# Kernel tuning notes

Hardware: AMD Instinct MI355X
Metric: run time of the kernel (lower is better)

Reference implementation:

```python
import jax, jax.numpy as jnp
import numpy as np

ALPHA_SIZE = 256
EMBED_DIM = 256
HIDDEN = 1024
BATCH = 64
SEQ = 512
TEMPERATURE = 1.0


def setup_inputs() -> dict:
    key = jax.random.key(0)
    ks = jax.random.split(key, 10)
    s = 0.05  # keep activations in a sane range
    return {
        "x": jax.random.randint(ks[0], (BATCH, SEQ), 0, ALPHA_SIZE, dtype=jnp.int32),
        "emb": jax.random.normal(ks[1], (ALPHA_SIZE, EMBED_DIM), jnp.float32) * s,
        "W0": jax.random.normal(ks[2], (EMBED_DIM, 3 * HIDDEN), jnp.float32) * s,
        "U0": jax.random.normal(ks[3], (HIDDEN, 3 * HIDDEN), jnp.float32) * s,
        "b0": jax.random.normal(ks[4], (2, 3 * HIDDEN), jnp.float32) * s,
        "W1": jax.random.normal(ks[5], (HIDDEN, 3 * HIDDEN), jnp.float32) * s,
        "U1": jax.random.normal(ks[6], (HIDDEN, 3 * HIDDEN), jnp.float32) * s,
        "b1": jax.random.normal(ks[7], (2, 3 * HIDDEN), jnp.float32) * s,
        "Wd": jax.random.normal(ks[8], (HIDDEN, ALPHA_SIZE), jnp.float32) * s,
        "bd": jax.random.normal(ks[9], (ALPHA_SIZE,), jnp.float32) * s,
        "training": 0,
    }


def gru_layer(x, W, U, b):
    # Keras GRU, reset_after=True, gate order (z, r, h). x: [B,S,D]
    B, S, _ = x.shape
    H = U.shape[0]
    # precompute input-side gates for all timesteps: [B,S,3H]
    xg = jnp.einsum("bsd,dg->bsg", x, W) + b[0]

    def step(h, xg_t):
        hg = h @ U + b[1]  # [B,3H]
        xz, xr, xh = jnp.split(xg_t, 3, axis=-1)
        hz, hr, hh_r = jnp.split(hg, 3, axis=-1)
        z = jax.nn.sigmoid(xz + hz)
        r = jax.nn.sigmoid(xr + hr)
        hh = jnp.tanh(xh + r * hh_r)
        h_new = z * h + (1.0 - z) * hh
        return h_new, h_new

    h0 = jnp.zeros((B, H), x.dtype)
    _, ys = jax.lax.scan(step, h0, jnp.swapaxes(xg, 0, 1))  # [S,B,H]
    return jnp.swapaxes(ys, 0, 1)  # [B,S,H]


def reference(x, emb, W0, U0, b0, W1, U1, b1, Wd, bd, training):
    h = emb[x]  # [B,S,E]
    h = gru_layer(h, W0, U0, b0)
    h = gru_layer(h, W1, U1, b1)
    logits = jnp.einsum("bsh,hv->bsv", h, Wd) + bd
    if not training:
        logits = logits / TEMPERATURE
    return jax.nn.softmax(logits, axis=-1)
```

## Files before the change

### kernel.cpp

```cpp
#include <hip/hip_runtime.h>

typedef _Float16 half_t;
typedef _Float16 half8 __attribute__((ext_vector_type(8)));
typedef _Float16 half4 __attribute__((ext_vector_type(4)));
typedef _Float16 half2 __attribute__((ext_vector_type(2)));
typedef float f32x4 __attribute__((ext_vector_type(4)));
typedef float f32x2 __attribute__((ext_vector_type(2)));

__global__ void wt_transpose(const float* __restrict__ in, half_t* __restrict__ outp,
                             int K, int N, int ldo, int co) {
  __shared__ float tile[32][33];
  int nb = blockIdx.x * 32, kb = blockIdx.y * 32;
  int tx = threadIdx.x, ty = threadIdx.y;
  for (int i = ty; i < 32; i += 8)
    tile[i][tx] = in[(size_t)(kb + i) * N + nb + tx];
  __syncthreads();
  for (int i = ty; i < 32; i += 8)
    outp[(size_t)(nb + i) * ldo + co + kb + tx] = (half_t)tile[tx][i];
}

__global__ __launch_bounds__(256) void embed_kernel(const int* __restrict__ x,
    const float* __restrict__ emb, half_t* __restrict__ E) {
  int g = blockIdx.x * 256 + threadIdx.x;
  int m = g >> 5, dp = g & 31;
  int b = m & 63, s = m >> 6;
  int tok = x[b * 512 + s];
  const float* src = emb + (size_t)tok * 256 + dp * 8;
  half8 v;
  #pragma unroll
  for (int i = 0; i < 8; ++i) v[i] = (half_t)src[i];
  *(half8*)(E + (size_t)m * 256 + dp * 8) = v;
}

__global__ __launch_bounds__(256)
void gemm128(const half_t* __restrict__ A, const half_t* __restrict__ BT,
             float* __restrict__ C, int N, int K) {
  __shared__ __align__(16) half_t As[128 * 32];
  __shared__ __align__(16) half_t Bs[128 * 32];
  const int tid = threadIdx.x;
  const int lane = tid & 63, wid = tid >> 6;
  const int wm = wid >> 1, wn = wid & 1;
  const int l15 = lane & 15, l4 = lane >> 4;
  const int bm = blockIdx.y * 128, bn = blockIdx.x * 128;
  const int srow = tid >> 2;
  const int skb = (tid & 3) * 8;
  f32x4 acc[4][4] = {};

  half8 va[2], vb[2];
  #pragma unroll
  for (int c = 0; c < 2; ++c) {
    int row = c * 64 + srow;
    va[c] = *(const half8*)(A + (size_t)(bm + row) * K + skb);
    vb[c] = *(const half8*)(BT + (size_t)(bn + row) * K + skb);
  }
  for (int k0 = 0; k0 < K; k0 += 32) {
    __syncthreads();
    #pragma unroll
    for (int c = 0; c < 2; ++c) {
      int row = c * 64 + srow;
      *(half8*)(As + row * 32 + skb) = va[c];
      *(half8*)(Bs + row * 32 + skb) = vb[c];
    }
    __syncthreads();
    int k1 = k0 + 32;
    if (k1 < K) {
      #pragma unroll
      for (int c = 0; c < 2; ++c) {
        int row = c * 64 + srow;
        va[c] = *(const half8*)(A + (size_t)(bm + row) * K + k1 + skb);
        vb[c] = *(const half8*)(BT + (size_t)(bn + row) * K + k1 + skb);
      }
    }
    half8 af[4], bf[4];
    #pragma unroll
    for (int mt = 0; mt < 4; ++mt)
      af[mt] = *(const half8*)(As + (wm * 64 + mt * 16 + l15) * 32 + l4 * 8);
    #pragma unroll
    for (int nt = 0; nt < 4; ++nt)
      bf[nt] = *(const half8*)(Bs + (wn * 64 + nt * 16 + l15) * 32 + l4 * 8);
    #pragma unroll
    for (int mt = 0; mt < 4; ++mt)
      #pragma unroll
      for (int nt = 0; nt < 4; ++nt)
        acc[mt][nt] = __builtin_amdgcn_mfma_f32_16x16x32_f16(af[mt], bf[nt], acc[mt][nt], 0, 0, 0);
  }
  #pragma unroll
  for (int mt = 0; mt < 4; ++mt)
    #pragma unroll
    for (int nt = 0; nt < 4; ++nt) {
      int col = bn + wn * 64 + nt * 16 + l15;
      int row0 = bm + wm * 64 + mt * 16 + l4 * 4;
      #pragma unroll
      for (int r = 0; r < 4; ++r)
        C[(size_t)(row0 + r) * N + col] = acc[mt][nt][r];
    }
}

#define MF(af, bf, a) a = __builtin_amdgcn_mfma_f32_16x16x32_f16(af, bf, a, 0, 0, 0)
#define BC8(x) __builtin_bit_cast(half8, x)
#define GLD4(dst, base, OFS) asm volatile("global_load_dwordx4 %0, %1, off offset:" OFS " sc0 sc1" : "=v"(dst) : "v"(base))
#define GLD4P(dst, base, OFS) asm volatile("global_load_dwordx4 %0, %1, off offset:" OFS : "=v"(dst) : "v"(base))
#define HL8(t, B) GLD4(hrA[t][0],B,"0");GLD4(hrA[t][1],B,"64");GLD4(hrA[t][2],B,"128");GLD4(hrA[t][3],B,"192");GLD4(hrA[t][4],B,"256");GLD4(hrA[t][5],B,"320");GLD4(hrA[t][6],B,"384");GLD4(hrA[t][7],B,"448")
#define HL16(t, B) HL8(t,B);GLD4(hrA[t][8],B,"512");GLD4(hrA[t][9],B,"576");GLD4(hrA[t][10],B,"640");GLD4(hrA[t][11],B,"704");GLD4(hrA[t][12],B,"768");GLD4(hrA[t][13],B,"832");GLD4(hrA[t][14],B,"896");GLD4(hrA[t][15],B,"960")
#define LDH0(u, kt) (*(const half8*)(smem + ((((u) * 2048) + wv * 512 + (kt) * 64 + l4x16) ^ (((u) & 7) << 4))))
#define LDE0(u, kt) (*(const half8*)(smem + 65536 + ((((u) * 512) + wv * 128 + (kt) * 64 + l4x16) ^ (((u) & 7) << 4))))
#define LDH1(kt) (*(const half8*)(smem + ((l15 * 4096 + wv * 1024 + (kt) * 64 + l4x16) ^ ((l15 & 7) << 4))))
#define SB __builtin_amdgcn_sched_barrier(0)

#define POLLC(fp, tgt, fsav) { int dm_ = 0; \
    while (!__all((fsav) >= (tgt))) { \
      if ((fsav) < (tgt)) \
        asm volatile("global_load_dword %0, %1, off sc0 sc1\n\ts_waitcnt vmcnt(0)" \
                     : "=v"(fsav) : "v"(fp) : "memory"); \
      if (++dm_ > (1 << 14)) break; \
    } }

__global__ __launch_bounds__(256, 1)
void recur_fused(const half_t* __restrict__ E16,
                 const half_t* __restrict__ T0,
                 const half_t* __restrict__ T1,
                 const float* __restrict__ bias0,
                 const float* __restrict__ bias1,
                 half_t* __restrict__ ys1,
                 half_t* __restrict__ h0f,
                 half_t* __restrict__ h1f,
                 int* __restrict__ flags0,
                 int* __restrict__ flags1) {
  extern __shared__ unsigned char smem[];
  const int tid = threadIdx.x;
  const int lane = tid & 63, wv = tid >> 6;
  const int l15 = lane & 15, l4 = lane >> 4;
  const int l4x16 = l4 * 16;
  const int ug = tid >> 5;
  const int bl = lane & 31;

  if (blockIdx.x < 64) {
    const int w = blockIdx.x;
    const int g = w >> 5, uslot = w & 31, j0 = uslot * 32;
    float* hgp = (float*)(smem + 81920);

    for (int it = 0; it < 16; ++it) {
      int idx = it * 256 + tid;
      int u = idx >> 7, kc = idx & 127;
      int byteoff = (u * 2048 + kc * 16) ^ ((u & 7) << 4);
      *(half8*)(smem + byteoff) =
          *(const half8*)(T0 + (size_t)(2048 + j0 + u) * 1280 + kc * 8);
    }
    for (int it = 0; it < 4; ++it) {
      int idx = it * 256 + tid;
      int u = idx >> 5, kc = idx & 31;
      int byteoff = 65536 + ((u * 512 + kc * 16) ^ ((u & 7) << 4));
      *(half8*)(smem + byteoff) =
          *(const half8*)(T0 + (size_t)(2048 + j0 + u) * 1280 + 1024 + kc * 8);
    }
    half8 zr[2][2][8], ezr[2][2][2];
    #pragma unroll
    for (int gate = 0; gate < 2; ++gate)
      #pragma unroll
      for (int uh = 0; uh < 2; ++uh) {
        const half_t* row = T0 + (size_t)(gate * 1024 + j0 + uh * 16 + l15) * 1280;
        #pragma unroll
        for (int kt = 0; kt < 8; ++kt)
          zr[gate][uh][kt] = *(const half8*)(row + wv * 256 + kt * 32 + l4 * 8);
        #pragma unroll
        for (int kt = 0; kt < 2; ++kt)
          ezr[gate][uh][kt] = *(const half8*)(row + 1024 + wv * 64 + kt * 32 + l4 * 8);
      }
    float bz[4], br[4], bhr[4], bxh[4], hM[4];
    #pragma unroll
    for (int q = 0; q < 4; ++q) {
      int j = j0 + ug * 4 + q;
      bz[q]  = bias0[j]        + bias0[3072 + j];
      br[q]  = bias0[1024 + j] + bias0[4096 + j];
      bxh[q] = bias0[2048 + j];
      bhr[q] = bias0[5120 + j];
      hM[q] = 0.f;
    }
    const int* fp = (lane < 32)
        ? flags0 + (wv * 64 + g * 32 + bl) * 4
        : flags1 + (wv * 128 + g * 64 + wv * 16 + (lane & 15)) * 4;
    int fsav0 = 0;
    f32x4 erC[2][2], erN[2][2];
    {
      const char* eb0 = (const char*)E16 + (size_t)(g * 32 + l15) * 512 + wv * 128 + l4x16;
      const char* eb1 = eb0 + 8192;
      GLD4P(erC[0][0], eb0, "0"); GLD4P(erC[0][1], eb0, "64");
      GLD4P(erC[1][0], eb1, "0"); GLD4P(erC[1][1], eb1, "64");
    }
    asm volatile("s_waitcnt vmcnt(0)" ::: "memory");
    __syncthreads();

    for (int e = 0; e < 512; ++e) {
      POLLC(fp, ((lane < 32) ? e : (e - 5)), fsav0);
      f32x4 hrA[2][8];
      {
        const char* hbb = (const char*)h0f + (size_t)((e + 5) % 6) * 131072;
        const char* hb0 = hbb + (g * 32 + l15) * 2048 + wv * 512 + l4x16;
        const char* hb1 = hb0 + 32768;
        HL8(0, hb0); HL8(1, hb1);
        int en = (e < 511) ? e + 1 : e;
        const char* eb0 = (const char*)E16 +
            (size_t)(en * 64 + g * 32 + l15) * 512 + wv * 128 + l4x16;
        const char* eb1 = eb0 + 8192;
        GLD4P(erN[0][0], eb0, "0"); GLD4P(erN[0][1], eb0, "64");
        GLD4P(erN[1][0], eb1, "0"); GLD4P(erN[1][1], eb1, "64");
      }
      asm volatile("s_waitcnt vmcnt(12)" ::: "memory"); SB;
      __builtin_amdgcn_s_setprio(1);
      f32x4 acc[2][8] = {};
      #pragma unroll
      for (int kt = 0; kt < 8; ++kt) {
        half8 af0 = BC8(hrA[0][kt]);
        MF(af0, zr[0][0][kt], acc[0][0]);
        MF(af0, zr[0][1][kt], acc[0][1]);
        MF(af0, zr[1][0][kt], acc[0][2]);
        MF(af0, zr[1][1][kt], acc[0][3]);
        half8 bh0 = LDH0(l15, kt), bh1 = LDH0(16 + l15, kt);
        MF(af0, bh0, acc[0][4]);
        MF(af0, bh1, acc[0][5]);
      }
      asm volatile("s_waitcnt vmcnt(4)" ::: "memory"); SB;
      #pragma unroll
      for (int kt = 0; kt < 8; ++kt) {
        half8 af1 = BC8(hrA[1][kt]);
        MF(af1, zr[0][0][kt], acc[1][0]);
        MF(af1, zr[0][1][kt], acc[1][1]);
        MF(af1, zr[1][0][kt], acc[1][2]);
        MF(af1, zr[1][1][kt], acc[1][3]);
        half8 bh0 = LDH0(l15, kt), bh1 = LDH0(16 + l15, kt);
        MF(af1, bh0, acc[1][4]);
        MF(af1, bh1, acc[1][5]);
      }
      asm volatile("s_waitcnt vmcnt(0)" ::: "memory"); SB;
      #pragma unroll
      for (int kt = 0; kt < 2; ++kt) {
        half8 af0 = BC8(erC[0][kt]), af1 = BC8(erC[1][kt]);
        MF(af0, ezr[0][0][kt], acc[0][0]); MF(af1, ezr[0][0][kt], acc[1][0]);
        MF(af0, ezr[0][1][kt], acc[0][1]); MF(af1, ezr[0][1][kt], acc[1][1]);
        MF(af0, ezr[1][0][kt], acc[0][2]); MF(af1, ezr[1][0][kt], acc[1][2]);
        MF(af0, ezr[1][1][kt], acc[0][3]); MF(af1, ezr[1][1][kt], acc[1][3]);
        half8 be0 = LDE0(l15, kt), be1 = LDE0(16 + l15, kt);
        MF(af0, be0, acc[0][6]); MF(af1, be0, acc[1][6]);
        MF(af0, be1, acc[0][7]); MF(af1, be1, acc[1][7]);
      }
      __builtin_amdgcn_s_setprio(0);
      #pragma unroll
      for (int m = 0; m < 2; ++m)
        #pragma unroll
        for (int n = 0; n < 8; ++n) {
          int colb = (n < 6) ? ((n >> 1) * 32 + (n & 1) * 16) : (96 + (n & 1) * 16);
          #pragma unroll
          for (int r = 0; r < 4; ++r)
            hgp[(wv * 32 + m * 16 + l4 * 4 + r) * 129 + colb + l15] = acc[m][n][r];
        }
      __syncthreads();
      half4 hv;
      #pragma unroll
      for (int q = 0; q < 4; ++q) {
        int c = ug * 4 + q;
        float hz = 0.f, hr = 0.f, hhh = 0.f, xh = 0.f;
        #pragma unroll
        for (int kv = 0; kv < 4; ++kv) {
          const float* rowp = hgp + (kv * 32 + bl) * 129 + c;
          hz += rowp[0]; hr += rowp[32]; hhh += rowp[64]; xh += rowp[96];
        }
        float z = 1.f / (1.f + __expf(-(hz + bz[q])));
        float r = 1.f / (1.f + __expf(-(hr + br[q])));
        float targ = xh + bxh[q] + r * (hhh + bhr[q]);
        float hh = 1.f - 2.f / (1.f + __expf(2.f * targ));
        float hnew = z * hM[q] + (1.f - z) * hh;
        hM[q] = hnew;
        hv[q] = (half_t)hnew;
      }
      #pragma unroll
      for (int a = 0; a < 2; ++a)
        #pragma unroll
        for (int b2 = 0; b2 < 2; ++b2) erC[a][b2] = erN[a][b2];
      {
        const char* dst = (const char*)h0f + (size_t)(e % 6) * 131072
                        + (g * 32 + bl) * 2048 + (j0 + ug * 4) * 2;
        f32x2 pv = __builtin_bit_cast(f32x2, hv);
        asm volatile("global_store_dwordx2 %0, %1, off sc0 sc1"
                     :: "v"(dst), "v"(pv) : "memory");
      }
      asm volatile("s_waitcnt vmcnt(0)" ::: "memory");
      __syncthreads();
      if (tid < 4) {
        int tv = e + 1;
        const int* dst = flags0 + (tid * 64 + w) * 4;
        asm volatile("global_store_dword %0, %1, off sc0 sc1"
                     :: "v"(dst), "v"(tv) : "memory");
      }
    }
  } else {
    const int wp = blockIdx.x - 64;
    const int g = wp >> 6, uslot = wp & 63, j0 = uslot * 16;
    float* hgp = (float*)(smem + 65536);

    for (int it = 0; it < 16; ++it) {
      int idx = it * 256 + tid;
      int u = idx >> 8, kc = idx & 255;
      int byteoff = (u * 4096 + kc * 16) ^ ((u & 7) << 4);
      *(half8*)(smem + byteoff) =
          *(const half8*)(T1 + (size_t)(2048 + j0 + u) * 2048 + kc * 8);
    }
    half8 zr1[2][16];
    #pragma unroll
    for (int gate = 0; gate < 2; ++gate) {
      const half_t* row = T1 + (size_t)(gate * 1024 + j0 + l15) * 2048 + wv * 512;
      #pragma unroll
      for (int kt = 0; kt < 16; ++kt)
        zr1[gate][kt] = *(const half8*)(row + kt * 32 + l4 * 8);
    }
    float bz[2], br[2], bhr[2], bxh[2], hM[2];
    #pragma unroll
    for (int q = 0; q < 2; ++q) {
      int j = j0 + ug * 2 + q;
      bz[q]  = bias1[j]        + bias1[3072 + j];
      br[q]  = bias1[1024 + j] + bias1[4096 + j];
      bxh[q] = bias1[2048 + j];
      bhr[q] = bias1[5120 + j];
      hM[q] = 0.f;
    }
    const int* fp = (wv < 2)
        ? flags0 + (wv * 64 + g * 32 + bl) * 4
        : flags1 + (wv * 128 + g * 64 + lane) * 4;
    int fsav1 = 0;
    __syncthreads();

    for (int e = 1; e <= 512; ++e) {
      POLLC(fp, ((wv < 2) ? e : (e - 1)), fsav1);
      f32x4 hrA[2][16];
      {
        const char* fb = (wv < 2)
            ? (const char*)h0f + (size_t)((e + 5) % 6) * 131072
            : (const char*)h1f + (size_t)((e + 2) & 3) * 131072;
        const char* b0 = fb + (g * 32 + l15) * 2048 + (wv & 1) * 1024 + l4x16;
        const char* b1 = b0 + 32768;
        HL16(0, b0); HL16(1, b1);
      }
      asm volatile("s_waitcnt vmcnt(16)" ::: "memory"); SB;
      __builtin_amdgcn_s_setprio(1);
      f32x4 acc[2][3] = {};
      #pragma unroll
      for (int kt = 0; kt < 16; ++kt) {
        half8 af0 = BC8(hrA[0][kt]);
        MF(af0, zr1[0][kt], acc[0][0]);
        MF(af0, zr1[1][kt], acc[0][1]);
        half8 bh = LDH1(kt);
        MF(af0, bh, acc[0][2]);
      }
      asm volatile("s_waitcnt vmcnt(0)" ::: "memory"); SB;
      #pragma unroll
      for (int kt = 0; kt < 16; ++kt) {
        half8 af1 = BC8(hrA[1][kt]);
        MF(af1, zr1[0][kt], acc[1][0]);
        MF(af1, zr1[1][kt], acc[1][1]);
        half8 bh = LDH1(kt);
        MF(af1, bh, acc[1][2]);
      }
      __builtin_amdgcn_s_setprio(0);
      {
        int hhcol = (wv < 2) ? 48 : 32;
        #pragma unroll
        for (int m = 0; m < 2; ++m)
          #pragma unroll
          for (int r = 0; r < 4; ++r) {
            int row = (wv * 32 + m * 16 + l4 * 4 + r) * 65;
            hgp[row + l15]        = acc[m][0][r];
            hgp[row + 16 + l15]   = acc[m][1][r];
            hgp[row + hhcol + l15] = acc[m][2][r];
          }
      }
      __syncthreads();
      half2 hv;
      #pragma unroll
      for (int q = 0; q < 2; ++q) {
        int c = ug * 2 + q;
        float hz = 0.f, hr = 0.f;
        #pragma unroll
        for (int kv = 0; kv < 4; ++kv) {
          const float* rowp = hgp + (kv * 32 + bl) * 65 + c;
          hz += rowp[0]; hr += rowp[16];
        }
        float hhh = hgp[(2 * 32 + bl) * 65 + 32 + c] + hgp[(3 * 32 + bl) * 65 + 32 + c];
        float xh  = hgp[(0 * 32 + bl) * 65 + 48 + c] + hgp[(1 * 32 + bl) * 65 + 48 + c];
        float z = 1.f / (1.f + __expf(-(hz + bz[q])));
        float r = 1.f / (1.f + __expf(-(hr + br[q])));
        float targ = xh + bxh[q] + r * (hhh + bhr[q]);
        float hh = 1.f - 2.f / (1.f + __expf(2.f * targ));
        float hnew = z * hM[q] + (1.f - z) * hh;
        hM[q] = hnew;
        hv[q] = (half_t)hnew;
      }
      *(half2*)(ys1 + ((size_t)(e - 1) * 64 + g * 32 + bl) * 1024 + j0 + ug * 2) = hv;
      {
        const char* dst = (const char*)h1f + (size_t)((e + 3) & 3) * 131072
                        + (g * 32 + bl) * 2048 + (j0 + ug * 2) * 2;
        float pv = __builtin_bit_cast(float, hv);
        asm volatile("global_store_dword %0, %1, off sc0 sc1"
                     :: "v"(dst), "v"(pv) : "memory");
      }
      asm volatile("s_waitcnt vmcnt(0)" ::: "memory");
      __syncthreads();
      if (tid < 4) {
        int tv = e;
        const int* dst = flags1 + (tid * 128 + wp) * 4;
        asm volatile("global_store_dword %0, %1, off sc0 sc1"
                     :: "v"(dst), "v"(tv) : "memory");
      }
    }
  }
}

__global__ __launch_bounds__(256)
void softmax_kernel(const float* __restrict__ logits, const float* __restrict__ bd,
                    float* __restrict__ out) {
  int w = threadIdx.x >> 6, lane = threadIdx.x & 63;
  int m = blockIdx.x * 4 + w;
  const float* lrow = logits + (size_t)m * 256;
  float v[4];
  #pragma unroll
  for (int i = 0; i < 4; ++i) v[i] = lrow[lane + i * 64] + bd[lane + i * 64];
  float mx = fmaxf(fmaxf(v[0], v[1]), fmaxf(v[2], v[3]));
  #pragma unroll
  for (int off = 32; off; off >>= 1) mx = fmaxf(mx, __shfl_xor(mx, off));
  float s = 0.f;
  #pragma unroll
  for (int i = 0; i < 4; ++i) { v[i] = __expf(v[i] - mx); s += v[i]; }
  #pragma unroll
  for (int off = 32; off; off >>= 1) s += __shfl_xor(s, off);
  float inv = 1.f / s;
  int b = m & 63, sq = m >> 6;
  float* orow = out + ((size_t)b * 512 + sq) * 256;
  #pragma unroll
  for (int i = 0; i < 4; ++i) orow[lane + i * 64] = v[i] * inv;
}

extern "C" void kernel_launch(void* const* d_in, const int* in_sizes, int n_in,
                              void* d_out, int out_size, void* d_ws, size_t ws_size,
                              hipStream_t stream) {
  const int*   x   = (const int*)d_in[0];
  const float* emb = (const float*)d_in[1];
  const float* W0  = (const float*)d_in[2];
  const float* U0  = (const float*)d_in[3];
  const float* b0  = (const float*)d_in[4];
  const float* W1  = (const float*)d_in[5];
  const float* U1  = (const float*)d_in[6];
  const float* b1  = (const float*)d_in[7];
  const float* Wd  = (const float*)d_in[8];
  const float* bd  = (const float*)d_in[9];
  float* out = (float*)d_out;
  (void)in_sizes; (void)n_in; (void)out_size; (void)ws_size;

  char* p = (char*)d_ws;
  size_t off = 0;
  auto take = [&](size_t bytes) {
    char* r = p + off;
    off = (off + bytes + 255) & ~(size_t)255;
    return r;
  };
  half_t* T0  = (half_t*)take(3072ull * 1280 * 2);
  half_t* T1  = (half_t*)take(3072ull * 2048 * 2);
  half_t* WdT = (half_t*)take(256ull * 1024 * 2);
  const size_t H0B = 6ull * 131072, H1B = 4ull * 131072;
  const size_t F0B = 4096, F1B = 8192;
  char* stateblk = take(H0B + H1B + F0B + F1B);
  half_t* h0f   = (half_t*)stateblk;
  half_t* h1f   = (half_t*)(stateblk + H0B);
  int*    flags0 = (int*)(stateblk + H0B + H1B);
  int*    flags1 = (int*)(stateblk + H0B + H1B + F0B);
  half_t* E16 = (half_t*)take(32768ull * 256 * 2);
  half_t* ys1 = (half_t*)take(32768ull * 1024 * 2);
  float* logits = (float*)take(32768ull * 256 * 4);

  wt_transpose<<<dim3(96, 32), dim3(32, 8), 0, stream>>>(U0, T0, 1024, 3072, 1280, 0);
  wt_transpose<<<dim3(96, 8),  dim3(32, 8), 0, stream>>>(W0, T0, 256,  3072, 1280, 1024);
  wt_transpose<<<dim3(96, 32), dim3(32, 8), 0, stream>>>(W1, T1, 1024, 3072, 2048, 0);
  wt_transpose<<<dim3(96, 32), dim3(32, 8), 0, stream>>>(U1, T1, 1024, 3072, 2048, 1024);
  wt_transpose<<<dim3(8, 32),  dim3(32, 8), 0, stream>>>(Wd, WdT, 1024, 256, 1024, 0);
  embed_kernel<<<4096, 256, 0, stream>>>(x, emb, E16);

  hipFuncSetAttribute((const void*)recur_fused,
                      hipFuncAttributeMaxDynamicSharedMemorySize, 147968);
  hipMemsetAsync(stateblk, 0, H0B + H1B + F0B + F1B, stream);

  recur_fused<<<192, 256, 147968, stream>>>(E16, T0, T1, b0, b1, ys1,
                                            h0f, h1f, flags0, flags1);

  gemm128<<<dim3(2, 256), 256, 0, stream>>>(ys1, WdT, logits, 256, 1024);
  softmax_kernel<<<8192, 256, 0, stream>>>(logits, bd, out);
}
```

Measured before the change: 3.587 ms.

## Use per-wave completion flags instead of block barrier before flag publish

```diff
diff --git a/kernel.cpp b/kernel.cpp
--- a/kernel.cpp
+++ b/kernel.cpp
@@ -106,14 +106,6 @@
 #define LDE0(u, kt) (*(const half8*)(smem + 65536 + ((((u) * 512) + wv * 128 + (kt) * 64 + l4x16) ^ (((u) & 7) << 4))))
 #define LDH1(kt) (*(const half8*)(smem + ((l15 * 4096 + wv * 1024 + (kt) * 64 + l4x16) ^ ((l15 & 7) << 4))))
 #define SB __builtin_amdgcn_sched_barrier(0)
-
-#define POLLC(fp, tgt, fsav) { int dm_ = 0; \
-    while (!__all((fsav) >= (tgt))) { \
-      if ((fsav) < (tgt)) \
-        asm volatile("global_load_dword %0, %1, off sc0 sc1\n\ts_waitcnt vmcnt(0)" \
-                     : "=v"(fsav) : "v"(fp) : "memory"); \
-      if (++dm_ > (1 << 14)) break; \
-    } }
 
 __global__ __launch_bounds__(256, 1)
 void recur_fused(const half_t* __restrict__ E16,
@@ -176,10 +168,11 @@
       bhr[q] = bias0[5120 + j];
       hM[q] = 0.f;
     }
-    const int* fp = (lane < 32)
-        ? flags0 + (wv * 64 + g * 32 + bl) * 4
-        : flags1 + (wv * 128 + g * 64 + wv * 16 + (lane & 15)) * 4;
-    int fsav0 = 0;
+    const int* pda = flags0 + (g * 128 + lane) * 4;
+    const int* pdb = flags0 + (g * 128 + 64 + lane) * 4;
+    const int* pwa = flags1 + ((g * 64 + lane) * 4 + 0) * 4;
+    const int* pwb = flags1 + ((g * 64 + lane) * 4 + 1) * 4;
+    int fda = 0, fdb = 0, fwa = 0, fwb = 0;
     f32x4 erC[2][2], erN[2][2];
     {
       const char* eb0 = (const char*)E16 + (size_t)(g * 32 + l15) * 512 + wv * 128 + l4x16;
@@ -191,7 +184,21 @@
     __syncthreads();
 
     for (int e = 0; e < 512; ++e) {
-      POLLC(fp, ((lane < 32) ? e : (e - 5)), fsav0);
+      {
+        int dm = 0;
+        while (!__all((fda >= e) & (fdb >= e) & (fwa >= e - 5) & (fwb >= e - 5))) {
+          asm volatile(
+            "global_load_dword %0, %4, off sc0 sc1\n\t"
+            "global_load_dword %1, %5, off sc0 sc1\n\t"
+            "global_load_dword %2, %6, off sc0 sc1\n\t"
+            "global_load_dword %3, %7, off sc0 sc1\n\t"
+            "s_waitcnt vmcnt(0)"
+            : "=v"(fda), "=v"(fdb), "=v"(fwa), "=v"(fwb)
+            : "v"(pda), "v"(pdb), "v"(pwa), "v"(pwb)
+            : "memory");
+          if (++dm > (1 << 14)) break;
+        }
+      }
       f32x4 hrA[2][8];
       {
         const char* hbb = (const char*)h0f + (size_t)((e + 5) % 6) * 131072;
@@ -284,10 +291,9 @@
                      :: "v"(dst), "v"(pv) : "memory");
       }
       asm volatile("s_waitcnt vmcnt(0)" ::: "memory");
-      __syncthreads();
-      if (tid < 4) {
+      if (lane == 0) {
         int tv = e + 1;
-        const int* dst = flags0 + (tid * 64 + w) * 4;
+        const int* dst = flags0 + (w * 4 + wv) * 4;
         asm volatile("global_store_dword %0, %1, off sc0 sc1"
                      :: "v"(dst), "v"(tv) : "memory");
       }
@@ -322,14 +328,33 @@
       bhr[q] = bias1[5120 + j];
       hM[q] = 0.f;
     }
-    const int* fp = (wv < 2)
-        ? flags0 + (wv * 64 + g * 32 + bl) * 4
-        : flags1 + (wv * 128 + g * 64 + lane) * 4;
-    int fsav1 = 0;
+    const int* pd = flags0 + (g * 128 + wv * 64 + lane) * 4;
+    const int wvx = (wv >= 2) ? (wv - 2) : 0;
+    const int pairbase = g * 256 + (wvx * 64 + lane) * 2;
+    const int* ps0 = flags1 + pairbase * 4;
+    const int* ps1 = flags1 + (pairbase + 1) * 4;
+    int fd = 0, fs0 = 0, fs1 = 0;
     __syncthreads();
 
     for (int e = 1; e <= 512; ++e) {
-      POLLC(fp, ((wv < 2) ? e : (e - 1)), fsav1);
+      if (wv < 2) {
+        int dm = 0;
+        while (!__all(fd >= e)) {
+          asm volatile("global_load_dword %0, %1, off sc0 sc1\n\ts_waitcnt vmcnt(0)"
+                       : "=v"(fd) : "v"(pd) : "memory");
+          if (++dm > (1 << 14)) break;
+        }
+      } else {
+        int dm = 0;
+        while (!__all((fs0 >= e - 1) & (fs1 >= e - 1))) {
+          asm volatile(
+            "global_load_dword %0, %2, off sc0 sc1\n\t"
+            "global_load_dword %1, %3, off sc0 sc1\n\t"
+            "s_waitcnt vmcnt(0)"
+            : "=v"(fs0), "=v"(fs1) : "v"(ps0), "v"(ps1) : "memory");
+          if (++dm > (1 << 14)) break;
+        }
+      }
       f32x4 hrA[2][16];
       {
         const char* fb = (wv < 2)
@@ -402,13 +427,13 @@
                      :: "v"(dst), "v"(pv) : "memory");
       }
       asm volatile("s_waitcnt vmcnt(0)" ::: "memory");
-      __syncthreads();
-      if (tid < 4) {
+      if (lane == 0) {
         int tv = e;
-        const int* dst = flags1 + (tid * 128 + wp) * 4;
+        const int* dst = flags1 + (wp * 4 + wv) * 4;
         asm volatile("global_store_dword %0, %1, off sc0 sc1"
                      :: "v"(dst), "v"(tv) : "memory");
       }
+      __syncthreads();
     }
   }
 }
```

Result: slower. 4.353 ms (+21.4%).
